# Kernel tuning notes

Measured on AMD Instinct MI355X. Metric: run time of the kernel, lower is better.

## Reference

```python
import jax, jax.numpy as jnp
import numpy as np

def setup_inputs() -> dict:
    key = jax.random.key(0)
    k1, k2, k3 = jax.random.split(key, 3)
    shape = (2, 2048, 8, 64)  # [n, l, h, d]
    return {
        "q": jax.random.normal(k1, shape, dtype=jnp.float32),
        "k": jax.random.normal(k2, shape, dtype=jnp.float32),
        "v": jax.random.normal(k3, shape, dtype=jnp.float32),
    }

def reference(q, k, v):
    # QK^T: [n, l, s, h]
    qk = jnp.einsum('nlhd,nshd->nlsh', q, k)
    softmax_temp = 1.0 / (q.shape[3] ** 0.5)
    attn = jax.nn.softmax(softmax_temp * qk, axis=2)
    # weighted values: [n, l, h, d]
    return jnp.einsum('nlsh,nshd->nlhd', attn, v)
```

## Files before the change

### kernel.cpp

```cpp
#include <hip/hip_runtime.h>
#include <hip/hip_bf16.h>
#include <math.h>

typedef float floatx16 __attribute__((ext_vector_type(16)));
typedef __bf16 bf16x8 __attribute__((ext_vector_type(8)));

#define SEQ 2048
#define NH 8
#define DH 64
#define NB 2
#define HEADS 16
#define HSTRIDE (SEQ * DH)
#define TILE_E (64 * 64)

__device__ __forceinline__ unsigned short f2bf(float x) {
  union { __bf16 b; unsigned short u; } c; c.b = (__bf16)x; return c.u;
}
__device__ __forceinline__ unsigned int pk2bf(float a, float b) {
  union { __hip_bfloat162 h2; unsigned int u; } c;
  c.h2 = __float22bfloat162_rn(make_float2(a, b));
  return c.u;
}

__device__ __forceinline__ void hswap_fwd(unsigned& a, unsigned& b) {
  asm volatile("v_permlane32_swap_b32 %0, %1" : "+v"(a), "+v"(b));
}
__device__ __forceinline__ void hswap_rev(unsigned& a, unsigned& b) {
  asm volatile("v_permlane32_swap_b32 %0, %1" : "+v"(b), "+v"(a));
}

__global__ __launch_bounds__(256)
void pack_kv(const float* __restrict__ k, const float* __restrict__ v,
             unsigned short* __restrict__ kb, unsigned short* __restrict__ vb) {
  __shared__ unsigned short Ts[64][68];
  const int tid  = threadIdx.x;
  const int bx   = blockIdx.x;
  const int kt   = bx & 31;
  const int head = bx >> 5;
  const int n = head >> 3, h = head & 7;

  #pragma unroll
  for (int j2 = 0; j2 < 2; ++j2) {
    int c = j2 * 256 + tid;
    int lane = c & 63;
    int kk = (c >> 6) & 3, ks2 = c >> 8;
    int row = kt * 64 + ks2 * 32 + (lane & 31);
    int d0  = kk * 16 + (lane >> 5) * 8;
    const float* src = k + ((size_t)(n * SEQ + row) * NH + h) * DH + d0;
    float4 a = *(const float4*)src;
    float4 b = *(const float4*)(src + 4);
    ushort4 lo, hi;
    lo.x = f2bf(a.x); lo.y = f2bf(a.y); lo.z = f2bf(a.z); lo.w = f2bf(a.w);
    hi.x = f2bf(b.x); hi.y = f2bf(b.y); hi.z = f2bf(b.z); hi.w = f2bf(b.w);
    unsigned short* dst = kb + (size_t)head * HSTRIDE + kt * TILE_E + c * 8;
    *(ushort4*)dst = lo;
    *(ushort4*)(dst + 4) = hi;
  }

  #pragma unroll
  for (int i = 0; i < 4; ++i) {
    int id = i * 256 + tid;
    int s  = id >> 4;
    int c4 = (id & 15) * 4;
    size_t g = ((size_t)((n * SEQ + kt * 64 + s) * NH + h)) * DH + c4;
    float4 x = *(const float4*)(v + g);
    ushort4 y;
    y.x = f2bf(x.x); y.y = f2bf(x.y); y.z = f2bf(x.z); y.w = f2bf(x.w);
    *(ushort4*)&Ts[s][c4] = y;
  }
  __syncthreads();
  #pragma unroll
  for (int j2 = 0; j2 < 2; ++j2) {
    int c = j2 * 256 + tid;
    int lane = c & 63;
    int dsub = (c >> 6) & 1, ss = c >> 7;
    int s0 = ss * 16 + (lane >> 5) * 8;
    int d  = dsub * 32 + (lane & 31);
    ushort4 lo, hi;
    lo.x = Ts[s0 + 0][d]; lo.y = Ts[s0 + 1][d]; lo.z = Ts[s0 + 2][d]; lo.w = Ts[s0 + 3][d];
    hi.x = Ts[s0 + 4][d]; hi.y = Ts[s0 + 5][d]; hi.z = Ts[s0 + 6][d]; hi.w = Ts[s0 + 7][d];
    unsigned short* dst = vb + (size_t)head * HSTRIDE + kt * TILE_E + c * 8;
    *(ushort4*)dst = lo;
    *(ushort4*)(dst + 4) = hi;
  }
}

#define SMEM_BYTES 35328

__global__ __launch_bounds__(512)
void attn(const float* __restrict__ q, const unsigned short* __restrict__ kb,
          const unsigned short* __restrict__ vt, float* __restrict__ out) {
  __shared__ __align__(16) char smem[SMEM_BYTES];
  float* oM = (float*)smem;
  float* lM = (float*)(smem + 8 * 16 * 68 * 4);

  const int tid  = threadIdx.x;
  const int wave = tid >> 6;
  const int lane = tid & 63;
  const int l32  = lane & 31;
  const int hl   = lane >> 5;

  unsigned px = (unsigned)lane, py = (unsigned)lane + 100u;
  hswap_fwd(px, py);
  const bool mir = (__builtin_amdgcn_readfirstlane(px) != 0u);

  const int bx   = blockIdx.x;
  const int head = bx & 15;
  const int qg   = bx >> 4;
  const int n = head >> 3, h = head & 7;

  const unsigned short* kf = kb + (size_t)head * HSTRIDE;
  const unsigned short* vf = vt + (size_t)head * HSTRIDE;

  bf16x8 qB[2][4];
  #pragma unroll
  for (int qs = 0; qs < 2; ++qs)
    #pragma unroll
    for (int kk = 0; kk < 4; ++kk) {
      const int row = qg * 64 + qs * 32 + l32;
      const float* src = q + ((size_t)((n * SEQ + row) * NH + h)) * DH + kk * 16 + hl * 8;
      float4 x0 = *(const float4*)src;
      float4 x1 = *(const float4*)(src + 4);
      union { unsigned int u32[4]; bf16x8 v8; } u;
      u.u32[0] = pk2bf(x0.x, x0.y); u.u32[1] = pk2bf(x0.z, x0.w);
      u.u32[2] = pk2bf(x1.x, x1.y); u.u32[3] = pk2bf(x1.z, x1.w);
      qB[qs][kk] = u.v8;
    }

  floatx16 o[2][2];
  float lsum[2];
  #pragma unroll
  for (int qs = 0; qs < 2; ++qs) {
    lsum[qs] = 0.f;
    #pragma unroll
    for (int d = 0; d < 2; ++d)
      #pragma unroll
      for (int i = 0; i < 16; ++i) o[qs][d][i] = 0.f;
  }

  const float S = 0.125f * 1.4426950408889634f;
  const float C = 12.0f;

  for (int it = 0; it < 4; ++it) {
    const int kt = it * 8 + wave;
    const unsigned short* kt_base = kf + kt * TILE_E;
    const unsigned short* vt_base = vf + kt * TILE_E;

    bf16x8 kA[2][4];
    #pragma unroll
    for (int ks2 = 0; ks2 < 2; ++ks2)
      #pragma unroll
      for (int kk = 0; kk < 4; ++kk)
        kA[ks2][kk] = *(const bf16x8*)(kt_base + ((ks2 * 4 + kk) * 64 + lane) * 8);
    bf16x8 vB[4][2];
    #pragma unroll
    for (int ss = 0; ss < 4; ++ss)
      #pragma unroll
      for (int dsub = 0; dsub < 2; ++dsub)
        vB[ss][dsub] = *(const bf16x8*)(vt_base + ((ss * 2 + dsub) * 64 + lane) * 8);

    #pragma unroll
    for (int ks2 = 0; ks2 < 2; ++ks2) {
      floatx16 acc2[2];
      #pragma unroll
      for (int i = 0; i < 16; ++i) acc2[0][i] = 0.f;
      #pragma unroll
      for (int kk = 0; kk < 4; ++kk)
        acc2[0] = __builtin_amdgcn_mfma_f32_32x32x16_bf16(kA[ks2][kk], qB[0][kk], acc2[0], 0, 0, 0);

      #pragma unroll
      for (int m = 0; m < 2; ++m) {
        unsigned pk[8];
        #pragma unroll
        for (int g2 = 0; g2 < 4; ++g2) {
          float p0 = __builtin_amdgcn_exp2f(acc2[m][4 * g2 + 0] * S - C);
          float p1 = __builtin_amdgcn_exp2f(acc2[m][4 * g2 + 1] * S - C);
          float p2 = __builtin_amdgcn_exp2f(acc2[m][4 * g2 + 2] * S - C);
          float p3 = __builtin_amdgcn_exp2f(acc2[m][4 * g2 + 3] * S - C);
          lsum[m] += (p0 + p1) + (p2 + p3);
          pk[g2 * 2]     = pk2bf(p0, p1);
          pk[g2 * 2 + 1] = pk2bf(p2, p3);
        }

        if (m == 0) {
          #pragma unroll
          for (int i = 0; i < 16; ++i) acc2[1][i] = 0.f;
          #pragma unroll
          for (int kk = 0; kk < 4; ++kk)
            acc2[1] = __builtin_amdgcn_mfma_f32_32x32x16_bf16(kA[ks2][kk], qB[1][kk], acc2[1], 0, 0, 0);
        }

        union { unsigned u32[4]; bf16x8 v8; } A1, A2;
        A1.u32[0] = pk[0]; A1.u32[2] = pk[2];
        A1.u32[1] = pk[1]; A1.u32[3] = pk[3];
        A2.u32[0] = pk[4]; A2.u32[2] = pk[6];
        A2.u32[1] = pk[5]; A2.u32[3] = pk[7];
        if (!mir) {
          hswap_fwd(A1.u32[0], A1.u32[2]); hswap_fwd(A1.u32[1], A1.u32[3]);
          hswap_fwd(A2.u32[0], A2.u32[2]); hswap_fwd(A2.u32[1], A2.u32[3]);
        } else {
          hswap_rev(A1.u32[0], A1.u32[2]); hswap_rev(A1.u32[1], A1.u32[3]);
          hswap_rev(A2.u32[0], A2.u32[2]); hswap_rev(A2.u32[1], A2.u32[3]);
        }

        o[m][0] = __builtin_amdgcn_mfma_f32_32x32x16_bf16(A1.v8, vB[ks2 * 2][0],     o[m][0], 0, 0, 0);
        o[m][1] = __builtin_amdgcn_mfma_f32_32x32x16_bf16(A1.v8, vB[ks2 * 2][1],     o[m][1], 0, 0, 0);
        o[m][0] = __builtin_amdgcn_mfma_f32_32x32x16_bf16(A2.v8, vB[ks2 * 2 + 1][0], o[m][0], 0, 0, 0);
        o[m][1] = __builtin_amdgcn_mfma_f32_32x32x16_bf16(A2.v8, vB[ks2 * 2 + 1][1], o[m][1], 0, 0, 0);
      }
    }
  }

  #pragma unroll
  for (int qs = 0; qs < 2; ++qs)
    lsum[qs] += __shfl_xor(lsum[qs], 32, 64);

  const int mrow = tid >> 5;
  const int mcol = (tid & 31) * 2;
  #pragma unroll
  for (int p = 0; p < 4; ++p) {
    const int qsub = p >> 1, rh = p & 1;
    __syncthreads();
    #pragma unroll
    for (int r8 = 0; r8 < 8; ++r8) {
      const int r   = rh * 8 + r8;
      const int rip = (r8 & 3) + 4 * hl + 8 * (r8 >> 2);
      oM[(wave * 16 + rip) * 68 + l32]      = o[qsub][0][r];
      oM[(wave * 16 + rip) * 68 + 32 + l32] = o[qsub][1][r];
    }
    if (lane < 32 && ((lane >> 4) & 1) == rh) lM[wave * 16 + (lane & 15)] = lsum[qsub];
    __syncthreads();
    float v0 = 0.f, v1 = 0.f, l = 0.f;
    #pragma unroll
    for (int w = 0; w < 8; ++w) {
      float2 t2 = *(const float2*)&oM[(w * 16 + mrow) * 68 + mcol];
      v0 += t2.x; v1 += t2.y;
      l += lM[w * 16 + mrow];
    }
    float inv = 1.f / l;
    const int grow = qg * 64 + p * 16 + mrow;
    float2 st; st.x = v0 * inv; st.y = v1 * inv;
    *(float2*)(out + ((size_t)((n * SEQ + grow) * NH + h)) * DH + mcol) = st;
  }
}

extern "C" void kernel_launch(void* const* d_in, const int* in_sizes, int n_in,
                              void* d_out, int out_size, void* d_ws, size_t ws_size,
                              hipStream_t stream) {
  const float* q = (const float*)d_in[0];
  const float* k = (const float*)d_in[1];
  const float* v = (const float*)d_in[2];
  float* out = (float*)d_out;
  (void)in_sizes; (void)n_in; (void)out_size; (void)ws_size;

  unsigned short* kb = (unsigned short*)d_ws;
  unsigned short* vb = kb + (size_t)HEADS * HSTRIDE;

  pack_kv<<<HEADS * (SEQ / 64), 256, 0, stream>>>(k, v, kb, vb);
  attn<<<HEADS * (SEQ / 64), 512, 0, stream>>>(q, kb, vb, out);
}
```

Measured before the change: 105.9 us.

## Split attention block waves into 2 query groups by 4 key groups

```diff
diff --git a/kernel.cpp b/kernel.cpp
--- a/kernel.cpp
+++ b/kernel.cpp
@@ -35,8 +35,8 @@
   __shared__ unsigned short Ts[64][68];
   const int tid  = threadIdx.x;
   const int bx   = blockIdx.x;
-  const int kt   = bx & 31;
-  const int head = bx >> 5;
+  const int head = bx & 15;
+  const int kt   = bx >> 4;
   const int n = head >> 3, h = head & 7;
 
   #pragma unroll
@@ -85,20 +85,22 @@
   }
 }
 
-#define SMEM_BYTES 35328
+#define SMEM_BYTES 37376
 
 __global__ __launch_bounds__(512)
 void attn(const float* __restrict__ q, const unsigned short* __restrict__ kb,
           const unsigned short* __restrict__ vt, float* __restrict__ out) {
   __shared__ __align__(16) char smem[SMEM_BYTES];
   float* oM = (float*)smem;
-  float* lM = (float*)(smem + 8 * 16 * 68 * 4);
+  float* lM = (float*)(smem + 8 * 16 * 72 * 4);
 
   const int tid  = threadIdx.x;
   const int wave = tid >> 6;
   const int lane = tid & 63;
   const int l32  = lane & 31;
   const int hl   = lane >> 5;
+  const int wq   = wave >> 2;
+  const int wk   = wave & 3;
 
   unsigned px = (unsigned)lane, py = (unsigned)lane + 100u;
   hswap_fwd(px, py);
@@ -106,7 +108,7 @@
 
   const int bx   = blockIdx.x;
   const int head = bx & 15;
-  const int qg   = bx >> 4;
+  const int qh2  = bx >> 4;
   const int n = head >> 3, h = head & 7;
 
   const unsigned short* kf = kb + (size_t)head * HSTRIDE;
@@ -117,7 +119,7 @@
   for (int qs = 0; qs < 2; ++qs)
     #pragma unroll
     for (int kk = 0; kk < 4; ++kk) {
-      const int row = qg * 64 + qs * 32 + l32;
+      const int row = qh2 * 128 + wq * 64 + qs * 32 + l32;
       const float* src = q + ((size_t)((n * SEQ + row) * NH + h)) * DH + kk * 16 + hl * 8;
       float4 x0 = *(const float4*)src;
       float4 x1 = *(const float4*)(src + 4);
@@ -141,8 +143,8 @@
   const float S = 0.125f * 1.4426950408889634f;
   const float C = 12.0f;
 
-  for (int it = 0; it < 4; ++it) {
-    const int kt = it * 8 + wave;
+  for (int it = 0; it < 8; ++it) {
+    const int kt = wk * 8 + it;
     const unsigned short* kt_base = kf + kt * TILE_E;
     const unsigned short* vt_base = vf + kt * TILE_E;
 
@@ -215,8 +217,10 @@
   for (int qs = 0; qs < 2; ++qs)
     lsum[qs] += __shfl_xor(lsum[qs], 32, 64);
 
-  const int mrow = tid >> 5;
-  const int mcol = (tid & 31) * 2;
+  const int r32  = tid >> 4;
+  const int wqr  = r32 >> 4;
+  const int prow = r32 & 15;
+  const int col4 = tid & 15;
   #pragma unroll
   for (int p = 0; p < 4; ++p) {
     const int qsub = p >> 1, rh = p & 1;
@@ -225,22 +229,24 @@
     for (int r8 = 0; r8 < 8; ++r8) {
       const int r   = rh * 8 + r8;
       const int rip = (r8 & 3) + 4 * hl + 8 * (r8 >> 2);
-      oM[(wave * 16 + rip) * 68 + l32]      = o[qsub][0][r];
-      oM[(wave * 16 + rip) * 68 + 32 + l32] = o[qsub][1][r];
+      oM[(wave * 16 + rip) * 72 + l32]      = o[qsub][0][r];
+      oM[(wave * 16 + rip) * 72 + 32 + l32] = o[qsub][1][r];
     }
     if (lane < 32 && ((lane >> 4) & 1) == rh) lM[wave * 16 + (lane & 15)] = lsum[qsub];
     __syncthreads();
-    float v0 = 0.f, v1 = 0.f, l = 0.f;
-    #pragma unroll
-    for (int w = 0; w < 8; ++w) {
-      float2 t2 = *(const float2*)&oM[(w * 16 + mrow) * 68 + mcol];
-      v0 += t2.x; v1 += t2.y;
-      l += lM[w * 16 + mrow];
+    float4 s = make_float4(0.f, 0.f, 0.f, 0.f);
+    float l = 0.f;
+    #pragma unroll
+    for (int j = 0; j < 4; ++j) {
+      const int w = wqr * 4 + j;
+      float4 t4 = *(const float4*)&oM[(w * 16 + prow) * 72 + col4 * 4];
+      s.x += t4.x; s.y += t4.y; s.z += t4.z; s.w += t4.w;
+      l += lM[w * 16 + prow];
     }
     float inv = 1.f / l;
-    const int grow = qg * 64 + p * 16 + mrow;
-    float2 st; st.x = v0 * inv; st.y = v1 * inv;
-    *(float2*)(out + ((size_t)((n * SEQ + grow) * NH + h)) * DH + mcol) = st;
+    const int grow = qh2 * 128 + wqr * 64 + p * 16 + prow;
+    float4 st; st.x = s.x * inv; st.y = s.y * inv; st.z = s.z * inv; st.w = s.w * inv;
+    *(float4*)(out + ((size_t)((n * SEQ + grow) * NH + h)) * DH + col4 * 4) = st;
   }
 }
 
@@ -257,5 +263,5 @@
   unsigned short* vb = kb + (size_t)HEADS * HSTRIDE;
 
   pack_kv<<<HEADS * (SEQ / 64), 256, 0, stream>>>(k, v, kb, vb);
-  attn<<<HEADS * (SEQ / 64), 512, 0, stream>>>(q, kb, vb, out);
-}
+  attn<<<HEADS * (SEQ / 128), 512, 0, stream>>>(q, kb, vb, out);
+}
```

Result: faster. 100.9 us (-4.7%).
